# Performance work log

Measured on AMD Instinct MI355X. Metric: run time of the kernel, lower is better.

Reference implementation:

```python
import jax, jax.numpy as jnp
import numpy as np

B, S, E = 512, 200, 128
NUM_C = 1024
DIFF = 100


def _glorot(k, shape):
    fan_in, fan_out = shape[-1], shape[0]
    lim = jnp.sqrt(6.0 / (fan_in + fan_out)).astype(jnp.float32)
    return jax.random.uniform(k, shape, jnp.float32, -lim, lim)


def setup_inputs() -> dict:
    key = jax.random.key(0)
    ks = jax.random.split(key, 16)
    c = jax.random.randint(ks[0], (B, S), 0, NUM_C + 1)
    sd = jax.random.randint(ks[1], (B, S), 0, DIFF + 2)
    a = jax.random.randint(ks[2], (B, S), 0, 2)
    cshft = jax.random.randint(ks[3], (B, S), 0, NUM_C + 1)
    sdshft = jax.random.randint(ks[4], (B, S), 0, DIFF + 2)
    # embedding tables (padding_idx=0 rows zeroed, as in nn.Embedding)
    c_table = _glorot(ks[5], (NUM_C + 1, E)).at[0].set(0.0)
    sd_table = _glorot(ks[6], (DIFF + 2, E)).at[0].set(0.0)
    a_table = _glorot(ks[7], (2, E))
    knowledge = _glorot(ks[8], (1, E))  # xavier_uniform [1, E]
    W1 = _glorot(ks[9], (E, 2 * E)); b1 = jnp.zeros((E,), jnp.float32)
    W2 = _glorot(ks[10], (E, E));     b2 = jnp.zeros((E,), jnp.float32)
    W3 = _glorot(ks[11], (E, E));     b3 = jnp.zeros((E,), jnp.float32)
    W4 = _glorot(ks[12], (E, 2 * E)); b4 = jnp.zeros((E,), jnp.float32)
    W5 = _glorot(ks[13], (E, 2 * E)); b5 = jnp.zeros((E,), jnp.float32)
    W6 = _glorot(ks[14], (E, 3 * E)); b6 = jnp.zeros((E,), jnp.float32)
    return dict(c=c, sd=sd, a=a, cshft=cshft, sdshft=sdshft,
                c_table=c_table, sd_table=sd_table, a_table=a_table,
                knowledge=knowledge,
                W1=W1, b1=b1, W2=W2, b2=b2, W3=W3, b3=b3,
                W4=W4, b4=b4, W5=W5, b5=b5, W6=W6, b6=b6)


def reference(c, sd, a, cshft, sdshft, c_table, sd_table, a_table, knowledge,
              W1, b1, W2, b2, W3, b3, W4, b4, W5, b5, W6, b6):
    # embedding lookups: [B, S, E]
    c_emb = c_table[c]
    sd_emb = sd_table[sd]
    a_emb = a_table[a]
    target_c = c_table[cshft]
    target_sd = sd_table[sdshft]

    input_data = jnp.concatenate((c_emb, sd_emb), -1) @ W1.T + b1      # [B,S,E]
    target_data = jnp.concatenate((target_c, target_sd), -1) @ W1.T + b1

    k0 = jnp.broadcast_to(knowledge, (c.shape[0], knowledge.shape[-1]))  # [B,E]

    def step(k, xs):
        sd_t, a_t, in_t = xs                       # each [B,E]
        qq = k - in_t
        gates_SDF = jax.nn.sigmoid(qq @ W2.T + b2)
        SDFt = gates_SDF * jnp.tanh(qq @ W3.T + b3)  # dropout = eval-mode identity
        x = jnp.concatenate((SDFt, a_t), -1)
        gates_PKA = jax.nn.sigmoid(x @ W4.T + b4)
        PKAt = gates_PKA * jnp.tanh(x @ W5.T + b5)
        ins = jnp.concatenate((k, a_t, sd_t), -1)
        gates_KSU = jax.nn.sigmoid(ins @ W6.T + b6)
        k_new = gates_KSU * k + (1.0 - gates_KSU) * PKAt
        return k_new, k_new

    xs = (jnp.swapaxes(sd_emb, 0, 1),      # [S,B,E]
          jnp.swapaxes(a_emb, 0, 1),
          jnp.swapaxes(input_data, 0, 1))
    _, hs = jax.lax.scan(step, k0, xs)     # hs: [S,B,E]
    output = jnp.swapaxes(hs, 0, 1)        # [B,S,E]

    logits = jnp.sum(target_data * output, axis=-1)  # [B,S]
    return jax.nn.sigmoid(logits)
```

## Files before the change

kernel.cpp:

```cpp
#include <hip/hip_runtime.h>


#define S_ 200
#define E_ 128
#define RS 136

typedef float  float4v __attribute__((ext_vector_type(4)));
typedef _Float16 f16x8 __attribute__((ext_vector_type(8)));

__device__ __forceinline__ float fast_sigmoid(float x) {
  return __builtin_amdgcn_rcpf(1.f + __expf(-x));
}
__device__ __forceinline__ float fast_tanh(float x) {
  return 2.f * __builtin_amdgcn_rcpf(1.f + __expf(-2.f * x)) - 1.f;
}

#define DPP_ADD(x, ctrl) \
  ((x) + __builtin_bit_cast(float, __builtin_amdgcn_update_dpp( \
       0, __builtin_bit_cast(int, (x)), (ctrl), 0xf, 0xf, true)))

__device__ __forceinline__ f16x8 cvt8(const float* __restrict__ p) {
  float4v a = *(const float4v*)p;
  float4v b = *(const float4v*)(p + 4);
  f16x8 r;
  r[0] = (_Float16)a[0]; r[1] = (_Float16)a[1];
  r[2] = (_Float16)a[2]; r[3] = (_Float16)a[3];
  r[4] = (_Float16)b[0]; r[5] = (_Float16)b[1];
  r[6] = (_Float16)b[2]; r[7] = (_Float16)b[3];
  return r;
}

__global__ __launch_bounds__(128) void dimkt_prep(
    const float* __restrict__ c_table, const float* __restrict__ sd_table,
    const float* __restrict__ a_table,
    const float* __restrict__ W1, const float* __restrict__ b1,
    const float* __restrict__ W4, const float* __restrict__ b4,
    const float* __restrict__ W5, const float* __restrict__ b5,
    const float* __restrict__ W6, const float* __restrict__ b6,
    float* __restrict__ ws) {
  __shared__ float s_src[E_];
  __shared__ float s_w[E_][33];
  const int row = blockIdx.x;
  const int t = threadIdx.x;
  const float* srcp; const float* wbase; int wstride, woff;
  const float* bias; float* dst;
  if (row < 1025)      {                  srcp = c_table + row * E_; wbase = W1; wstride = 256; woff = 0;   bias = nullptr; dst = ws + row * E_; }
  else if (row < 1127) { int i = row-1025; srcp = sd_table + i * E_; wbase = W1; wstride = 256; woff = 128; bias = b1;     dst = ws + 131200 + i * E_; }
  else if (row < 1229) { int i = row-1127; srcp = sd_table + i * E_; wbase = W6; wstride = 384; woff = 256; bias = nullptr; dst = ws + 144256 + i * E_; }
  else if (row < 1231) { int i = row-1229; srcp = a_table + i * E_;  wbase = W4; wstride = 256; woff = 128; bias = b4;     dst = ws + 157312 + i * E_; }
  else if (row < 1233) { int i = row-1231; srcp = a_table + i * E_;  wbase = W5; wstride = 256; woff = 128; bias = b5;     dst = ws + 157568 + i * E_; }
  else                 { int i = row-1233; srcp = a_table + i * E_;  wbase = W6; wstride = 384; woff = 128; bias = b6;     dst = ws + 157824 + i * E_; }
  s_src[t] = srcp[t];
  float acc = bias ? bias[t] : 0.f;
  for (int k0 = 0; k0 < 128; k0 += 32) {
    __syncthreads();
    const int jj = t & 31, eb = t >> 5;
    #pragma unroll 8
    for (int i = 0; i < 32; ++i) {
      int ee = i * 4 + eb;
      s_w[ee][jj] = wbase[ee * wstride + woff + k0 + jj];
    }
    __syncthreads();
    #pragma unroll 8
    for (int kk = 0; kk < 32; ++kk)
      acc += s_w[t][kk] * s_src[k0 + kk];
  }
  dst[t] = acc;
}

__global__ __launch_bounds__(512, 2) void dimkt_scan(
    const int* __restrict__ c, const int* __restrict__ sd, const int* __restrict__ a,
    const int* __restrict__ cshft, const int* __restrict__ sdshft,
    const float* __restrict__ knowledge,
    const float* __restrict__ W2, const float* __restrict__ b2,
    const float* __restrict__ W3, const float* __restrict__ b3,
    const float* __restrict__ W4, const float* __restrict__ W5,
    const float* __restrict__ W6,
    const float* __restrict__ ws, float* __restrict__ out) {

  const float* __restrict__ C1  = ws;
  const float* __restrict__ SD1 = ws + 131200;
  const float* __restrict__ SD6 = ws + 144256;
  const float* __restrict__ A4  = ws + 157312;
  const float* __restrict__ A5  = ws + 157568;
  const float* __restrict__ A6  = ws + 157824;

  const int tid  = threadIdx.x;
  const int w    = tid >> 6;
  const int lane = tid & 63;
  const int l15  = lane & 15;
  const int q    = lane >> 4;
  const int qodd = q & 1;
  const int e    = w * 16 + l15;
  const int j    = q >> 1;
  const int bj   = blockIdx.x * 2 + j;
  const int mrow = q << 2;

  __shared__ __attribute__((aligned(16))) _Float16 A1[16 * RS];
  __shared__ __attribute__((aligned(16))) _Float16 A2[16 * RS];
  __shared__ float red[8][2];

  for (int i = tid; i < 16 * RS; i += 512) { A1[i] = (_Float16)0.f; A2[i] = (_Float16)0.f; }

  const int st_off = mrow * RS + ((e + (q << 4)) & 127);
  int rdt[4];
  #pragma unroll
  for (int t = 0; t < 4; ++t)
    rdt[t] = l15 * RS + ((((4 * t + q) << 3) + ((l15 >> 2) << 4)) & 127);

  f16x8 w2f[4], w3f[4], w4f[4], w5f[4], w6f[4];
  #pragma unroll
  for (int t = 0; t < 4; ++t) {
    const int ko = t * 32 + q * 8;
    w2f[t] = cvt8(W2 + e * 128 + ko);
    w3f[t] = cvt8(W3 + e * 128 + ko);
    w4f[t] = cvt8(W4 + e * 256 + ko);
    w5f[t] = cvt8(W5 + e * 256 + ko);
    w6f[t] = cvt8(W6 + e * 384 + ko);
  }
  const float b2e = b2[e], b3e = b3[e];
  const float A4t0 = A4[e], A4t1 = A4[E_ + e];
  const float A5t0 = A5[e], A5t1 = A5[E_ + e];
  const float A6t0 = A6[e], A6t1 = A6[E_ + e];

  float kreg = knowledge[e];

  const int base = bj * S_;
  int ic = c[base], isd = sd[base], ia = a[base], ict = cshft[base], ist = sdshft[base];
  float inT  = C1[ic * E_ + e] + SD1[isd * E_ + e];
  float sd6v = SD6[isd * E_ + e];
  float a4v = ia ? A4t1 : A4t0;
  float a5v = ia ? A5t1 : A5t0;
  float a6v = ia ? A6t1 : A6t0;
  float tgt  = C1[ict * E_ + e] + SD1[ist * E_ + e];
  int nic = c[base + 1], nisd = sd[base + 1], nia = a[base + 1],
      nict = cshft[base + 1], nist = sdshft[base + 1];

  __syncthreads();
  A1[st_off] = (_Float16)(qodd ? kreg : (kreg - inT));
  __syncthreads();

  float4v acc2{0.f,0.f,0.f,0.f}, acc3{0.f,0.f,0.f,0.f}, acc6{0.f,0.f,0.f,0.f};
  float4v acc4{0.f,0.f,0.f,0.f}, acc5{0.f,0.f,0.f,0.f};

  #pragma unroll 1
  for (int s = 0; s < S_; ++s) {
    f16x8 f0 = *(const f16x8*)&A1[rdt[0]];
    f16x8 f1 = *(const f16x8*)&A1[rdt[1]];
    f16x8 f2 = *(const f16x8*)&A1[rdt[2]];
    f16x8 f3 = *(const f16x8*)&A1[rdt[3]];

    float ninT = C1[nic * E_ + e] + SD1[nisd * E_ + e];
    float nsd6 = SD6[nisd * E_ + e];
    float na4 = nia ? A4t1 : A4t0;
    float na5 = nia ? A5t1 : A5t0;
    float na6 = nia ? A6t1 : A6t0;
    float ntg  = C1[nict * E_ + e] + SD1[nist * E_ + e];

    acc2[0] = b2e;
    acc3[0] = b3e;
    acc6[0] = a6v + sd6v;
    acc2 = __builtin_amdgcn_mfma_f32_16x16x32_f16(f0, w2f[0], acc2, 0, 0, 0);
    acc3 = __builtin_amdgcn_mfma_f32_16x16x32_f16(f0, w3f[0], acc3, 0, 0, 0);
    acc6 = __builtin_amdgcn_mfma_f32_16x16x32_f16(f0, w6f[0], acc6, 0, 0, 0);
    acc2 = __builtin_amdgcn_mfma_f32_16x16x32_f16(f1, w2f[1], acc2, 0, 0, 0);
    acc3 = __builtin_amdgcn_mfma_f32_16x16x32_f16(f1, w3f[1], acc3, 0, 0, 0);
    acc6 = __builtin_amdgcn_mfma_f32_16x16x32_f16(f1, w6f[1], acc6, 0, 0, 0);
    acc2 = __builtin_amdgcn_mfma_f32_16x16x32_f16(f2, w2f[2], acc2, 0, 0, 0);
    acc3 = __builtin_amdgcn_mfma_f32_16x16x32_f16(f2, w3f[2], acc3, 0, 0, 0);
    acc6 = __builtin_amdgcn_mfma_f32_16x16x32_f16(f2, w6f[2], acc6, 0, 0, 0);
    acc2 = __builtin_amdgcn_mfma_f32_16x16x32_f16(f3, w2f[3], acc2, 0, 0, 0);
    acc3 = __builtin_amdgcn_mfma_f32_16x16x32_f16(f3, w3f[3], acc3, 0, 0, 0);
    acc6 = __builtin_amdgcn_mfma_f32_16x16x32_f16(f3, w6f[3], acc6, 0, 0, 0);

    int s2 = (s + 2 < S_) ? (s + 2) : (S_ - 1);
    int pi = bj * S_ + s2;
    int tic = c[pi], tisd = sd[pi], tia = a[pi], tict = cshft[pi], tist = sdshft[pi];

    const float xs  = qodd ? acc6[0] : acc2[0];
    const float g   = fast_sigmoid(xs);
    const float th3 = fast_tanh(acc3[0]);
    const float sdfv = g * th3;
    if (!qodd) A2[st_off] = (_Float16)sdfv;
    __syncthreads();

    f16x8 s0 = *(const f16x8*)&A2[rdt[0]];
    f16x8 s1 = *(const f16x8*)&A2[rdt[1]];
    f16x8 s2f = *(const f16x8*)&A2[rdt[2]];
    f16x8 s3 = *(const f16x8*)&A2[rdt[3]];

    acc4[0] = a4v;
    acc5[0] = a5v;
    acc4 = __builtin_amdgcn_mfma_f32_16x16x32_f16(s0, w4f[0], acc4, 0, 0, 0);
    acc5 = __builtin_amdgcn_mfma_f32_16x16x32_f16(s0, w5f[0], acc5, 0, 0, 0);
    acc4 = __builtin_amdgcn_mfma_f32_16x16x32_f16(s1, w4f[1], acc4, 0, 0, 0);
    acc5 = __builtin_amdgcn_mfma_f32_16x16x32_f16(s1, w5f[1], acc5, 0, 0, 0);
    acc4 = __builtin_amdgcn_mfma_f32_16x16x32_f16(s2f, w4f[2], acc4, 0, 0, 0);
    acc5 = __builtin_amdgcn_mfma_f32_16x16x32_f16(s2f, w5f[2], acc5, 0, 0, 0);
    acc4 = __builtin_amdgcn_mfma_f32_16x16x32_f16(s3, w4f[3], acc4, 0, 0, 0);
    acc5 = __builtin_amdgcn_mfma_f32_16x16x32_f16(s3, w5f[3], acc5, 0, 0, 0);

    const float pka = fast_sigmoid(acc4[0]) * fast_tanh(acc5[0]);
    const float send = qodd ? g : pka;
    const float recv = __shfl_xor(send, 16);
    const float gg6  = qodd ? g : recv;
    const float ppka = qodd ? recv : pka;
    const float knew = ppka + gg6 * (kreg - ppka);
    kreg = knew;
    A1[st_off] = (_Float16)(qodd ? knew : (knew - ninT));

    float p = tgt * knew;
    p = DPP_ADD(p, 0x111);
    p = DPP_ADD(p, 0x112);
    p = DPP_ADD(p, 0x114);
    p = DPP_ADD(p, 0x118);
    if (l15 == 15 && !qodd) red[w][j] = p;

    inT = ninT; sd6v = nsd6; a4v = na4; a5v = na5; a6v = na6; tgt = ntg;
    nic = tic; nisd = tisd; nia = tia; nict = tict; nist = tist;

    __syncthreads();

    if (tid == 0 || tid == 32) {
      const int jj = tid >> 5;
      float logit = 0.f;
      #pragma unroll
      for (int x = 0; x < 8; ++x) logit += red[x][jj];
      out[(blockIdx.x * 2 + jj) * S_ + s] = fast_sigmoid(logit);
    }
  }
}

extern "C" void kernel_launch(void* const* d_in, const int* in_sizes, int n_in,
                              void* d_out, int out_size, void* d_ws, size_t ws_size,
                              hipStream_t stream) {
  const int*   c         = (const int*)  d_in[0];
  const int*   sd        = (const int*)  d_in[1];
  const int*   a         = (const int*)  d_in[2];
  const int*   cshft     = (const int*)  d_in[3];
  const int*   sdshft    = (const int*)  d_in[4];
  const float* c_table   = (const float*)d_in[5];
  const float* sd_table  = (const float*)d_in[6];
  const float* a_table   = (const float*)d_in[7];
  const float* knowledge = (const float*)d_in[8];
  const float* W1 = (const float*)d_in[9];  const float* b1 = (const float*)d_in[10];
  const float* W2 = (const float*)d_in[11]; const float* b2 = (const float*)d_in[12];
  const float* W3 = (const float*)d_in[13]; const float* b3 = (const float*)d_in[14];
  const float* W4 = (const float*)d_in[15]; const float* b4 = (const float*)d_in[16];
  const float* W5 = (const float*)d_in[17]; const float* b5 = (const float*)d_in[18];
  const float* W6 = (const float*)d_in[19]; const float* b6 = (const float*)d_in[20];
  float* ws  = (float*)d_ws;
  float* out = (float*)d_out;
  (void)in_sizes; (void)n_in; (void)out_size; (void)ws_size;

  dimkt_prep<<<1235, 128, 0, stream>>>(c_table, sd_table, a_table,
                                       W1, b1, W4, b4, W5, b5, W6, b6, ws);
  dimkt_scan<<<256, 512, 0, stream>>>(c, sd, a, cshft, sdshft, knowledge,
                                      W2, b2, W3, b3, W4, W5, W6, ws, out);
}
```

Measured before the change: 277.6 us.

## Rework scan LDS operand layout to drop lane shuffle; batch prep rows per block

The prep kernel now computes 8 table rows per 256-thread block instead of one row per 128-thread block. This reuses each staged weight tile across several rows and cuts the grid from 1235 blocks to 158. In the scan kernel, the MFMA A-operand layout changes so every lane holds both the W2/W3 and W6 results. This removes the cross-lane shuffle and the select logic in the state update, at the cost of redundant index loads for both sequences per lane and extra LDS stores of the state.

```diff
diff --git a/kernel.cpp b/kernel.cpp
--- a/kernel.cpp
+++ b/kernel.cpp
@@ -30,7 +30,7 @@
   return r;
 }
 
-__global__ __launch_bounds__(128) void dimkt_prep(
+__global__ __launch_bounds__(256) void dimkt_prep(
     const float* __restrict__ c_table, const float* __restrict__ sd_table,
     const float* __restrict__ a_table,
     const float* __restrict__ W1, const float* __restrict__ b1,
@@ -38,34 +38,47 @@
     const float* __restrict__ W5, const float* __restrict__ b5,
     const float* __restrict__ W6, const float* __restrict__ b6,
     float* __restrict__ ws) {
-  __shared__ float s_src[E_];
+  __shared__ __attribute__((aligned(16))) float s_src[8][E_];
   __shared__ float s_w[E_][33];
-  const int row = blockIdx.x;
-  const int t = threadIdx.x;
-  const float* srcp; const float* wbase; int wstride, woff;
-  const float* bias; float* dst;
-  if (row < 1025)      {                  srcp = c_table + row * E_; wbase = W1; wstride = 256; woff = 0;   bias = nullptr; dst = ws + row * E_; }
-  else if (row < 1127) { int i = row-1025; srcp = sd_table + i * E_; wbase = W1; wstride = 256; woff = 128; bias = b1;     dst = ws + 131200 + i * E_; }
-  else if (row < 1229) { int i = row-1127; srcp = sd_table + i * E_; wbase = W6; wstride = 384; woff = 256; bias = nullptr; dst = ws + 144256 + i * E_; }
-  else if (row < 1231) { int i = row-1229; srcp = a_table + i * E_;  wbase = W4; wstride = 256; woff = 128; bias = b4;     dst = ws + 157312 + i * E_; }
-  else if (row < 1233) { int i = row-1231; srcp = a_table + i * E_;  wbase = W5; wstride = 256; woff = 128; bias = b5;     dst = ws + 157568 + i * E_; }
-  else                 { int i = row-1233; srcp = a_table + i * E_;  wbase = W6; wstride = 384; woff = 128; bias = b6;     dst = ws + 157824 + i * E_; }
-  s_src[t] = srcp[t];
-  float acc = bias ? bias[t] : 0.f;
-  for (int k0 = 0; k0 < 128; k0 += 32) {
-    __syncthreads();
-    const int jj = t & 31, eb = t >> 5;
-    #pragma unroll 8
-    for (int i = 0; i < 32; ++i) {
-      int ee = i * 4 + eb;
-      s_w[ee][jj] = wbase[ee * wstride + woff + k0 + jj];
-    }
-    __syncthreads();
-    #pragma unroll 8
-    for (int kk = 0; kk < 32; ++kk)
-      acc += s_w[t][kk] * s_src[k0 + kk];
-  }
-  dst[t] = acc;
+  const int blk = blockIdx.x, t = threadIdx.x;
+  const int e = t & 127, h = t >> 7;
+  const float* src; const float* wb; const float* bias; float* dst;
+  int r0, maxrow, wstr, woff;
+  if (blk < 129)      { r0 = blk * 8;       src = c_table;  maxrow = 1024; wb = W1; wstr = 256; woff = 0;   bias = nullptr; dst = ws; }
+  else if (blk < 142) { r0 = (blk-129) * 8; src = sd_table; maxrow = 101;  wb = W1; wstr = 256; woff = 128; bias = b1;      dst = ws + 131200; }
+  else if (blk < 155) { r0 = (blk-142) * 8; src = sd_table; maxrow = 101;  wb = W6; wstr = 384; woff = 256; bias = nullptr; dst = ws + 144256; }
+  else if (blk == 155){ r0 = 0;             src = a_table;  maxrow = 1;    wb = W4; wstr = 256; woff = 128; bias = b4;      dst = ws + 157312; }
+  else if (blk == 156){ r0 = 0;             src = a_table;  maxrow = 1;    wb = W5; wstr = 256; woff = 128; bias = b5;      dst = ws + 157568; }
+  else                { r0 = 0;             src = a_table;  maxrow = 1;    wb = W6; wstr = 384; woff = 128; bias = b6;      dst = ws + 157824; }
+  #pragma unroll
+  for (int i = 0; i < 4; ++i) {
+    int idx = i * 256 + t, row = idx >> 7, col = idx & 127;
+    int rr = r0 + row; if (rr > maxrow) rr = maxrow;
+    s_src[row][col] = src[rr * E_ + col];
+  }
+  float binit = bias ? bias[e] : 0.f;
+  float acc[4] = {binit, binit, binit, binit};
+  for (int k0 = 0; k0 < 4; ++k0) {
+    __syncthreads();
+    #pragma unroll
+    for (int i = 0; i < 16; ++i) {
+      int idx = i * 256 + t;
+      s_w[idx >> 5][idx & 31] = wb[(idx >> 5) * wstr + woff + k0 * 32 + (idx & 31)];
+    }
+    __syncthreads();
+    #pragma unroll 4
+    for (int kk = 0; kk < 32; ++kk) {
+      float wv = s_w[e][kk];
+      #pragma unroll
+      for (int g = 0; g < 4; ++g)
+        acc[g] += wv * s_src[h * 4 + g][k0 * 32 + kk];
+    }
+  }
+  #pragma unroll
+  for (int g = 0; g < 4; ++g) {
+    int row = r0 + h * 4 + g;
+    if (row <= maxrow) dst[row * E_ + e] = acc[g];
+  }
 }
 
 __global__ __launch_bounds__(512, 2) void dimkt_scan(
@@ -93,8 +106,6 @@
   const int qodd = q & 1;
   const int e    = w * 16 + l15;
   const int j    = q >> 1;
-  const int bj   = blockIdx.x * 2 + j;
-  const int mrow = q << 2;
 
   __shared__ __attribute__((aligned(16))) _Float16 A1[16 * RS];
   __shared__ __attribute__((aligned(16))) _Float16 A2[16 * RS];
@@ -102,11 +113,9 @@
 
   for (int i = tid; i < 16 * RS; i += 512) { A1[i] = (_Float16)0.f; A2[i] = (_Float16)0.f; }
 
-  const int st_off = mrow * RS + ((e + (q << 4)) & 127);
-  int rdt[4];
-  #pragma unroll
-  for (int t = 0; t < 4; ++t)
-    rdt[t] = l15 * RS + ((((4 * t + q) << 3) + ((l15 >> 2) << 4)) & 127);
+  const int stq = (j * 8) * RS + e;
+  const int stk = stq + RS;
+  int rd0 = l15 * RS + q * 8;
 
   f16x8 w2f[4], w3f[4], w4f[4], w5f[4], w6f[4];
   #pragma unroll
@@ -125,19 +134,36 @@
 
   float kreg = knowledge[e];
 
-  const int base = bj * S_;
-  int ic = c[base], isd = sd[base], ia = a[base], ict = cshft[base], ist = sdshft[base];
-  float inT  = C1[ic * E_ + e] + SD1[isd * E_ + e];
-  float sd6v = SD6[isd * E_ + e];
-  float a4v = ia ? A4t1 : A4t0;
-  float a5v = ia ? A5t1 : A5t0;
-  float a6v = ia ? A6t1 : A6t0;
-  float tgt  = C1[ict * E_ + e] + SD1[ist * E_ + e];
-  int nic = c[base + 1], nisd = sd[base + 1], nia = a[base + 1],
-      nict = cshft[base + 1], nist = sdshft[base + 1];
+  const int base0 = (blockIdx.x * 2) * S_, base1 = base0 + S_;
+  int ic0  = c[base0],      ic1  = c[base1];
+  int isd0 = sd[base0],     isd1 = sd[base1];
+  int ia0  = a[base0],      ia1  = a[base1];
+  int ict0 = cshft[base0],  ict1 = cshft[base1];
+  int ist0 = sdshft[base0], ist1 = sdshft[base1];
+
+  int sic  = j ? ic1  : ic0;
+  int sisd = j ? isd1 : isd0;
+  int sia  = j ? ia1  : ia0;
+  int sict = j ? ict1 : ict0;
+  int sist = j ? ist1 : ist0;
+  float inT  = C1[sic * E_ + e] + SD1[sisd * E_ + e];
+  float sd6v = SD6[sisd * E_ + e];
+  float a4v = sia ? A4t1 : A4t0;
+  float a5v = sia ? A5t1 : A5t0;
+  float a6v = sia ? A6t1 : A6t0;
+  float tgt  = C1[sict * E_ + e] + SD1[sist * E_ + e];
+
+  int nic0  = c[base0 + 1],      nic1  = c[base1 + 1];
+  int nisd0 = sd[base0 + 1],     nisd1 = sd[base1 + 1];
+  int nia0  = a[base0 + 1],      nia1  = a[base1 + 1];
+  int nict0 = cshft[base0 + 1],  nict1 = cshft[base1 + 1];
+  int nist0 = sdshft[base0 + 1], nist1 = sdshft[base1 + 1];
 
   __syncthreads();
-  A1[st_off] = (_Float16)(qodd ? kreg : (kreg - inT));
+  if (!qodd) {
+    A1[stq] = (_Float16)(kreg - inT);
+    A1[stk] = (_Float16)kreg;
+  }
   __syncthreads();
 
   float4v acc2{0.f,0.f,0.f,0.f}, acc3{0.f,0.f,0.f,0.f}, acc6{0.f,0.f,0.f,0.f};
@@ -145,21 +171,26 @@
 
   #pragma unroll 1
   for (int s = 0; s < S_; ++s) {
-    f16x8 f0 = *(const f16x8*)&A1[rdt[0]];
-    f16x8 f1 = *(const f16x8*)&A1[rdt[1]];
-    f16x8 f2 = *(const f16x8*)&A1[rdt[2]];
-    f16x8 f3 = *(const f16x8*)&A1[rdt[3]];
-
-    float ninT = C1[nic * E_ + e] + SD1[nisd * E_ + e];
-    float nsd6 = SD6[nisd * E_ + e];
-    float na4 = nia ? A4t1 : A4t0;
-    float na5 = nia ? A5t1 : A5t0;
-    float na6 = nia ? A6t1 : A6t0;
-    float ntg  = C1[nict * E_ + e] + SD1[nist * E_ + e];
+    f16x8 f0 = *(const f16x8*)&A1[rd0];
+    f16x8 f1 = *(const f16x8*)&A1[rd0 + 32];
+    f16x8 f2 = *(const f16x8*)&A1[rd0 + 64];
+    f16x8 f3 = *(const f16x8*)&A1[rd0 + 96];
+
+    int xic  = j ? nic1  : nic0;
+    int xisd = j ? nisd1 : nisd0;
+    int xia  = j ? nia1  : nia0;
+    int xict = j ? nict1 : nict0;
+    int xist = j ? nist1 : nist0;
+    float ninT = C1[xic * E_ + e] + SD1[xisd * E_ + e];
+    float nsd6 = SD6[xisd * E_ + e];
+    float na4 = xia ? A4t1 : A4t0;
+    float na5 = xia ? A5t1 : A5t0;
+    float na6 = xia ? A6t1 : A6t0;
+    float ntg  = C1[xict * E_ + e] + SD1[xist * E_ + e];
 
     acc2[0] = b2e;
     acc3[0] = b3e;
-    acc6[0] = a6v + sd6v;
+    acc6[1] = a6v + sd6v;
     acc2 = __builtin_amdgcn_mfma_f32_16x16x32_f16(f0, w2f[0], acc2, 0, 0, 0);
     acc3 = __builtin_amdgcn_mfma_f32_16x16x32_f16(f0, w3f[0], acc3, 0, 0, 0);
     acc6 = __builtin_amdgcn_mfma_f32_16x16x32_f16(f0, w6f[0], acc6, 0, 0, 0);
@@ -174,40 +205,42 @@
     acc6 = __builtin_amdgcn_mfma_f32_16x16x32_f16(f3, w6f[3], acc6, 0, 0, 0);
 
     int s2 = (s + 2 < S_) ? (s + 2) : (S_ - 1);
-    int pi = bj * S_ + s2;
-    int tic = c[pi], tisd = sd[pi], tia = a[pi], tict = cshft[pi], tist = sdshft[pi];
-
-    const float xs  = qodd ? acc6[0] : acc2[0];
-    const float g   = fast_sigmoid(xs);
+    int tic0  = c[base0 + s2],      tic1  = c[base1 + s2];
+    int tisd0 = sd[base0 + s2],     tisd1 = sd[base1 + s2];
+    int tia0  = a[base0 + s2],      tia1  = a[base1 + s2];
+    int tict0 = cshft[base0 + s2],  tict1 = cshft[base1 + s2];
+    int tist0 = sdshft[base0 + s2], tist1 = sdshft[base1 + s2];
+
+    const float g2  = fast_sigmoid(acc2[0]);
     const float th3 = fast_tanh(acc3[0]);
-    const float sdfv = g * th3;
-    if (!qodd) A2[st_off] = (_Float16)sdfv;
-    __syncthreads();
-
-    f16x8 s0 = *(const f16x8*)&A2[rdt[0]];
-    f16x8 s1 = *(const f16x8*)&A2[rdt[1]];
-    f16x8 s2f = *(const f16x8*)&A2[rdt[2]];
-    f16x8 s3 = *(const f16x8*)&A2[rdt[3]];
+    const float g6  = fast_sigmoid(acc6[1]);
+    const float sdfv = g2 * th3;
+    if (!qodd) A2[stq] = (_Float16)sdfv;
+    __syncthreads();
+
+    f16x8 g0 = *(const f16x8*)&A2[rd0];
+    f16x8 g1 = *(const f16x8*)&A2[rd0 + 32];
+    f16x8 g2f = *(const f16x8*)&A2[rd0 + 64];
+    f16x8 g3 = *(const f16x8*)&A2[rd0 + 96];
 
     acc4[0] = a4v;
     acc5[0] = a5v;
-    acc4 = __builtin_amdgcn_mfma_f32_16x16x32_f16(s0, w4f[0], acc4, 0, 0, 0);
-    acc5 = __builtin_amdgcn_mfma_f32_16x16x32_f16(s0, w5f[0], acc5, 0, 0, 0);
-    acc4 = __builtin_amdgcn_mfma_f32_16x16x32_f16(s1, w4f[1], acc4, 0, 0, 0);
-    acc5 = __builtin_amdgcn_mfma_f32_16x16x32_f16(s1, w5f[1], acc5, 0, 0, 0);
-    acc4 = __builtin_amdgcn_mfma_f32_16x16x32_f16(s2f, w4f[2], acc4, 0, 0, 0);
-    acc5 = __builtin_amdgcn_mfma_f32_16x16x32_f16(s2f, w5f[2], acc5, 0, 0, 0);
-    acc4 = __builtin_amdgcn_mfma_f32_16x16x32_f16(s3, w4f[3], acc4, 0, 0, 0);
-    acc5 = __builtin_amdgcn_mfma_f32_16x16x32_f16(s3, w5f[3], acc5, 0, 0, 0);
-
-    const float pka = fast_sigmoid(acc4[0]) * fast_tanh(acc5[0]);
-    const float send = qodd ? g : pka;
-    const float recv = __shfl_xor(send, 16);
-    const float gg6  = qodd ? g : recv;
-    const float ppka = qodd ? recv : pka;
-    const float knew = ppka + gg6 * (kreg - ppka);
+    acc4 = __builtin_amdgcn_mfma_f32_16x16x32_f16(g0, w4f[0], acc4, 0, 0, 0);
+    acc5 = __builtin_amdgcn_mfma_f32_16x16x32_f16(g0, w5f[0], acc5, 0, 0, 0);
+    acc4 = __builtin_amdgcn_mfma_f32_16x16x32_f16(g1, w4f[1], acc4, 0, 0, 0);
+    acc5 = __builtin_amdgcn_mfma_f32_16x16x32_f16(g1, w5f[1], acc5, 0, 0, 0);
+    acc4 = __builtin_amdgcn_mfma_f32_16x16x32_f16(g2f, w4f[2], acc4, 0, 0, 0);
+    acc5 = __builtin_amdgcn_mfma_f32_16x16x32_f16(g2f, w5f[2], acc5, 0, 0, 0);
+    acc4 = __builtin_amdgcn_mfma_f32_16x16x32_f16(g3, w4f[3], acc4, 0, 0, 0);
+    acc5 = __builtin_amdgcn_mfma_f32_16x16x32_f16(g3, w5f[3], acc5, 0, 0, 0);
+
+    const float pka  = fast_sigmoid(acc4[0]) * fast_tanh(acc5[0]);
+    const float knew = pka + g6 * (kreg - pka);
     kreg = knew;
-    A1[st_off] = (_Float16)(qodd ? knew : (knew - ninT));
+    if (!qodd) {
+      A1[stq] = (_Float16)(knew - ninT);
+      A1[stk] = (_Float16)knew;
+    }
 
     float p = tgt * knew;
     p = DPP_ADD(p, 0x111);
@@ -217,7 +250,9 @@
     if (l15 == 15 && !qodd) red[w][j] = p;
 
     inT = ninT; sd6v = nsd6; a4v = na4; a5v = na5; a6v = na6; tgt = ntg;
-    nic = tic; nisd = tisd; nia = tia; nict = tict; nist = tist;
+    nic0 = tic0;  nic1 = tic1;  nisd0 = tisd0; nisd1 = tisd1;
+    nia0 = tia0;  nia1 = tia1;  nict0 = tict0; nict1 = tict1;
+    nist0 = tist0; nist1 = tist1;
 
     __syncthreads();
 
@@ -253,8 +288,8 @@
   float* out = (float*)d_out;
   (void)in_sizes; (void)n_in; (void)out_size; (void)ws_size;
 
-  dimkt_prep<<<1235, 128, 0, stream>>>(c_table, sd_table, a_table,
-                                       W1, b1, W4, b4, W5, b5, W6, b6, ws);
+  dimkt_prep<<<158, 256, 0, stream>>>(c_table, sd_table, a_table,
+                                      W1, b1, W4, b4, W5, b5, W6, b6, ws);
   dimkt_scan<<<256, 512, 0, stream>>>(c, sd, a, cshft, sdshft, knowledge,
                                       W2, b2, W3, b3, W4, W5, W6, ws, out);
 }
```

After: 282.6 us. No clear change (+1.8%).
